# Performance work log

Hardware: AMD Instinct MI355X
Metric: run time of the kernel (lower is better)

## Reference

```python
import jax, jax.numpy as jnp
import numpy as np

B, N, F, R, DEG, STEPS = 4, 1024, 128, 16, 16, 2


def setup_inputs() -> dict:
    key = jax.random.key(0)
    ks = jax.random.split(key, 12)
    BN = B * N
    E = BN * DEG

    def edges(k):
        # edges kept within each graph of size N, then offset per graph
        e = jax.random.randint(k, (2, E), 0, N)
        off = jnp.repeat(jnp.arange(B, dtype=jnp.int32) * N, N * DEG)
        return e + off[None, :]

    return {
        "x_s": jax.random.normal(ks[0], (BN, F), jnp.float32),
        "edge_index_s": edges(ks[1]),
        "x_t": jax.random.normal(ks[2], (BN, F), jnp.float32),
        "edge_index_t": edges(ks[3]),
        "W1_self": jax.random.normal(ks[4], (F, F), jnp.float32) / np.float32(np.sqrt(F)),
        "W1_nbr": jax.random.normal(ks[5], (F, F), jnp.float32) / np.float32(np.sqrt(F)),
        "b1": jnp.zeros((F,), jnp.float32),
        "W2_self": jax.random.normal(ks[6], (R, R), jnp.float32) / np.float32(np.sqrt(R)),
        "W2_nbr": jax.random.normal(ks[7], (R, R), jnp.float32) / np.float32(np.sqrt(R)),
        "b2": jnp.zeros((R,), jnp.float32),
        "Wm1": jax.random.normal(ks[8], (R, R), jnp.float32) / np.float32(np.sqrt(R)),
        "bm1": jnp.zeros((R,), jnp.float32),
        "Wm2": jax.random.normal(ks[9], (R, 1), jnp.float32) / np.float32(np.sqrt(R)),
        "bm2": jnp.zeros((1,), jnp.float32),
        "r_steps": jax.random.normal(ks[10], (STEPS, B, N, R), jnp.float32),
    }


def _psi(x, ei, Ws, Wn, b):
    # simple GraphConv: self transform + summed neighbor transform
    agg = jax.ops.segment_sum(x[ei[0]], ei[1], num_segments=x.shape[0])
    return jax.nn.relu(x @ Ws + agg @ Wn + b)


def reference(x_s, edge_index_s, x_t, edge_index_t, W1_self, W1_nbr, b1,
              W2_self, W2_nbr, b2, Wm1, bm1, Wm2, bm2, r_steps):
    # psi_1 on both graphs, then dense-batch to [B, N, F] (equal-size graphs,
    # so masks are all-True and masked_softmax == softmax)
    h_s = _psi(x_s, edge_index_s, W1_self, W1_nbr, b1).reshape(B, N, F)
    h_t = _psi(x_t, edge_index_t, W1_self, W1_nbr, b1).reshape(B, N, F)

    S_hat = jnp.einsum('bsf,btf->bst', h_s, h_t)  # [B, Ns, Nt]
    S_0 = jax.nn.softmax(S_hat, axis=-1)

    for i in range(STEPS):
        S = jax.nn.softmax(S_hat, axis=-1)
        r_s = r_steps[i]                             # [B, N, R]
        r_t = jnp.einsum('bst,bsr->btr', S, r_s)     # S^T @ r_s
        o_s = _psi(r_s.reshape(B * N, R), edge_index_s, W2_self, W2_nbr, b2).reshape(B, N, R)
        o_t = _psi(r_t.reshape(B * N, R), edge_index_t, W2_self, W2_nbr, b2).reshape(B, N, R)
        D = o_s[:, :, None, :] - o_t[:, None, :, :]  # [B, Ns, Nt, R]
        upd = (jax.nn.relu(D @ Wm1 + bm1) @ Wm2 + bm2)[..., 0]
        S_hat = S_hat + upd

    S_L = jax.nn.softmax(S_hat, axis=-1)
    return (S_0, S_L)
```

## Files before the change

kernel.cpp:

```cpp
#include <hip/hip_runtime.h>

#define B_ 4
#define N_ 1024
#define F_ 128
#define R_ 16
#define E_ 65536
#define BN_ 4096

__global__ __launch_bounds__(256) void hist_k(
    const int* __restrict__ eis, const int* __restrict__ eit, int* __restrict__ counts) {
  const int* ei = blockIdx.y ? eit : eis;
  int* c = counts + blockIdx.y * BN_;
  int e = blockIdx.x * 256 + threadIdx.x;
  atomicAdd(c + ei[E_ + e], 1);
}

__global__ __launch_bounds__(256) void csr_scan(
    const int* __restrict__ counts, int* __restrict__ offs, int* __restrict__ cursor) {
  const int* c = counts + blockIdx.x * BN_;
  int* o = offs + blockIdx.x * (BN_ + 1);
  int* cur = cursor + blockIdx.x * BN_;
  int tid = threadIdx.x;
  int base = tid * 16;
  int local[16], sum = 0;
#pragma unroll
  for (int i = 0; i < 16; i++) { local[i] = sum; sum += c[base + i]; }
  __shared__ int csum[256];
  csum[tid] = sum;
  __syncthreads();
  for (int d = 1; d < 256; d <<= 1) {
    int v = (tid >= d) ? csum[tid - d] : 0;
    __syncthreads();
    csum[tid] += v;
    __syncthreads();
  }
  int prev = (tid == 0) ? 0 : csum[tid - 1];
#pragma unroll
  for (int i = 0; i < 16; i++) { int off = prev + local[i]; o[base + i] = off; cur[base + i] = off; }
  if (tid == 255) o[BN_] = csum[255];
}

__global__ __launch_bounds__(256) void csr_fill(
    const int* __restrict__ eis, const int* __restrict__ eit,
    int* __restrict__ cursor, int* __restrict__ csr) {
  const int* ei = blockIdx.y ? eit : eis;
  int* cur = cursor + blockIdx.y * BN_;
  int* cs = csr + blockIdx.y * E_;
  int e = blockIdx.x * 256 + threadIdx.x;
  int src = ei[e], dst = ei[E_ + e];
  int pos = atomicAdd(cur + dst, 1);
  cs[pos] = src;
}

__global__ __launch_bounds__(256) void gather_f(
    const float* __restrict__ xs, const float* __restrict__ xt,
    const int* __restrict__ csr, const int* __restrict__ offs,
    float* __restrict__ aggs, float* __restrict__ aggt) {
  const float* x = blockIdx.y ? xt : xs;
  const int* cs = csr + blockIdx.y * E_;
  const int* of = offs + blockIdx.y * (BN_ + 1);
  float* agg = blockIdx.y ? aggt : aggs;
  int node = blockIdx.x * 2 + (threadIdx.x >> 7);
  int ch = threadIdx.x & 127;
  int j0 = of[node], j1 = of[node + 1];
  float a0 = 0.f, a1 = 0.f, a2 = 0.f, a3 = 0.f;
  int j = j0;
  for (; j + 3 < j1; j += 4) {
    int s0 = cs[j], s1 = cs[j + 1], s2 = cs[j + 2], s3 = cs[j + 3];
    a0 += x[(size_t)s0 * F_ + ch];
    a1 += x[(size_t)s1 * F_ + ch];
    a2 += x[(size_t)s2 * F_ + ch];
    a3 += x[(size_t)s3 * F_ + ch];
  }
  for (; j < j1; j++) a0 += x[(size_t)cs[j] * F_ + ch];
  agg[(size_t)node * F_ + ch] = (a0 + a1) + (a2 + a3);
}

__global__ __launch_bounds__(256) void psi1_gemm(
    const float* __restrict__ xs, const float* __restrict__ aggs,
    const float* __restrict__ xt, const float* __restrict__ aggt,
    const float* __restrict__ Ws, const float* __restrict__ Wn,
    const float* __restrict__ bias, float* __restrict__ hs, float* __restrict__ ht) {
  const float* x   = blockIdx.z ? xt   : xs;
  const float* agg = blockIdx.z ? aggt : aggs;
  float*       h   = blockIdx.z ? ht   : hs;
  int n0 = blockIdx.x * 64, m0 = blockIdx.y * 64;
  int tid = threadIdx.x, tx = tid & 15, ty = tid >> 4;
  __shared__ __align__(16) float sA[16][68];
  __shared__ __align__(16) float sB[16][68];
  float acc[4][4] = {};
  for (int phase = 0; phase < 2; phase++) {
    const float* A  = phase ? agg : x;
    const float* Bw = phase ? Wn  : Ws;
    for (int kb = 0; kb < F_; kb += 16) {
      int row = tid >> 2, k4 = (tid & 3) * 4;
      float4 va = *(const float4*)(A + (size_t)(m0 + row) * F_ + kb + k4);
      sA[k4 + 0][row] = va.x; sA[k4 + 1][row] = va.y;
      sA[k4 + 2][row] = va.z; sA[k4 + 3][row] = va.w;
      int k = tid >> 4, n4 = (tid & 15) * 4;
      *(float4*)&sB[k][n4] = *(const float4*)(Bw + (size_t)(kb + k) * F_ + n0 + n4);
      __syncthreads();
#pragma unroll
      for (int kk = 0; kk < 16; kk++) {
        float a[4], bb[4];
        *(float4*)a  = *(const float4*)&sA[kk][ty * 4];
        *(float4*)bb = *(const float4*)&sB[kk][tx * 4];
#pragma unroll
        for (int i = 0; i < 4; i++)
#pragma unroll
          for (int j = 0; j < 4; j++) acc[i][j] += a[i] * bb[j];
      }
      __syncthreads();
    }
  }
  float4 bv = *(const float4*)(bias + n0 + tx * 4);
  float bj[4] = {bv.x, bv.y, bv.z, bv.w};
#pragma unroll
  for (int i = 0; i < 4; i++) {
    int m = m0 + ty * 4 + i;
    float4 o;
    o.x = fmaxf(acc[i][0] + bj[0], 0.f); o.y = fmaxf(acc[i][1] + bj[1], 0.f);
    o.z = fmaxf(acc[i][2] + bj[2], 0.f); o.w = fmaxf(acc[i][3] + bj[3], 0.f);
    *(float4*)(h + (size_t)m * F_ + n0 + tx * 4) = o;
  }
}

__global__ __launch_bounds__(256) void shat_gemm(
    const float* __restrict__ hs, const float* __restrict__ ht, float* __restrict__ S) {
  int b = blockIdx.z;
  int n0 = blockIdx.x * 128, m0 = blockIdx.y * 128;
  int tid = threadIdx.x, tx = tid & 15, ty = tid >> 4;
  __shared__ __align__(16) float sA[16][132];
  __shared__ __align__(16) float sB[16][132];
  float acc[8][8] = {};
  const float* Ag = hs + (size_t)(b * N_ + m0) * F_;
  const float* Bg = ht + (size_t)(b * N_ + n0) * F_;
  for (int kb = 0; kb < F_; kb += 16) {
#pragma unroll
    for (int l = 0; l < 2; l++) {
      int idx = tid + l * 256;
      int row = idx >> 2, k4 = (idx & 3) * 4;
      float4 va = *(const float4*)(Ag + (size_t)row * F_ + kb + k4);
      sA[k4 + 0][row] = va.x; sA[k4 + 1][row] = va.y;
      sA[k4 + 2][row] = va.z; sA[k4 + 3][row] = va.w;
      float4 vb = *(const float4*)(Bg + (size_t)row * F_ + kb + k4);
      sB[k4 + 0][row] = vb.x; sB[k4 + 1][row] = vb.y;
      sB[k4 + 2][row] = vb.z; sB[k4 + 3][row] = vb.w;
    }
    __syncthreads();
#pragma unroll
    for (int kk = 0; kk < 16; kk++) {
      float a[8], bb[8];
      *(float4*)&a[0]  = *(const float4*)&sA[kk][ty * 8];
      *(float4*)&a[4]  = *(const float4*)&sA[kk][ty * 8 + 4];
      *(float4*)&bb[0] = *(const float4*)&sB[kk][tx * 8];
      *(float4*)&bb[4] = *(const float4*)&sB[kk][tx * 8 + 4];
#pragma unroll
      for (int i = 0; i < 8; i++)
#pragma unroll
        for (int j = 0; j < 8; j++) acc[i][j] += a[i] * bb[j];
    }
    __syncthreads();
  }
#pragma unroll
  for (int i = 0; i < 8; i++) {
    size_t off = ((size_t)(b * N_ + m0 + ty * 8 + i)) * N_ + n0 + tx * 8;
    float4 o0 = {acc[i][0], acc[i][1], acc[i][2], acc[i][3]};
    float4 o1 = {acc[i][4], acc[i][5], acc[i][6], acc[i][7]};
    *(float4*)(S + off) = o0; *(float4*)(S + off + 4) = o1;
  }
}

__global__ __launch_bounds__(256) void softmax_row(
    const float* __restrict__ in, float* __restrict__ out) {
  int row = blockIdx.x;
  float4 v = ((const float4*)(in + (size_t)row * N_))[threadIdx.x];
  float m = fmaxf(fmaxf(v.x, v.y), fmaxf(v.z, v.w));
#pragma unroll
  for (int o = 32; o > 0; o >>= 1) m = fmaxf(m, __shfl_down(m, o, 64));
  __shared__ float rmax[4], rsum[4];
  int wave = threadIdx.x >> 6, lane = threadIdx.x & 63;
  if (lane == 0) rmax[wave] = m;
  __syncthreads();
  m = fmaxf(fmaxf(rmax[0], rmax[1]), fmaxf(rmax[2], rmax[3]));
  float e0 = __expf(v.x - m), e1 = __expf(v.y - m);
  float e2 = __expf(v.z - m), e3 = __expf(v.w - m);
  float s = e0 + e1 + e2 + e3;
#pragma unroll
  for (int o = 32; o > 0; o >>= 1) s += __shfl_down(s, o, 64);
  if (lane == 0) rsum[wave] = s;
  __syncthreads();
  s = rsum[0] + rsum[1] + rsum[2] + rsum[3];
  float inv = 1.f / s;
  float4 o4 = {e0 * inv, e1 * inv, e2 * inv, e3 * inv};
  ((float4*)(out + (size_t)row * N_))[threadIdx.x] = o4;
}

template <bool EXP>
__global__ __launch_bounds__(256) void rt_part_k(
    const float* __restrict__ S, const float2* __restrict__ stats,
    const float* __restrict__ rs, float* __restrict__ part) {
  int b = blockIdx.z, c = blockIdx.y, t0 = blockIdx.x * 256;
  int tid = threadIdx.x;
  int s0 = c * 32;
  __shared__ float rsh[32][16];
  __shared__ float sstat[64];
  if (tid < 128) {
    int srow = tid >> 2, c4 = (tid & 3) * 4;
    float4 v = *(const float4*)(rs + ((size_t)(b * N_ + s0 + srow)) * R_ + c4);
    rsh[srow][c4] = v.x; rsh[srow][c4 + 1] = v.y;
    rsh[srow][c4 + 2] = v.z; rsh[srow][c4 + 3] = v.w;
  } else if (EXP && tid < 192) {
    sstat[tid - 128] = ((const float*)(stats + b * N_ + s0))[tid - 128];
  }
  __syncthreads();
  float acc[16] = {};
  const float* Sp = S + ((size_t)(b * N_ + s0)) * N_ + t0 + tid;
#pragma unroll
  for (int s = 0; s < 32; s++) {
    float sv = Sp[(size_t)s * N_];
    if (EXP) sv = __expf(sv - sstat[2 * s]) * sstat[2 * s + 1];
#pragma unroll
    for (int r = 0; r < 16; r++) acc[r] += sv * rsh[s][r];
  }
  float* o = part + ((size_t)((b * 32 + c) * N_) + t0 + tid) * R_;
  *(float4*)(o + 0)  = *(float4*)&acc[0];
  *(float4*)(o + 4)  = *(float4*)&acc[4];
  *(float4*)(o + 8)  = *(float4*)&acc[8];
  *(float4*)(o + 12) = *(float4*)&acc[12];
}

__global__ __launch_bounds__(256) void rt_reduce(
    const float* __restrict__ part, float* __restrict__ rt) {
  int gid = blockIdx.x * 256 + threadIdx.x;
  int b = gid >> 12, tr = gid & 4095;
  const float* p = part + (size_t)b * (32 * N_ * R_) + (size_t)tr * 4;
  float4 acc = {0.f, 0.f, 0.f, 0.f};
#pragma unroll
  for (int c = 0; c < 32; c++) {
    float4 v = *(const float4*)(p + (size_t)c * (N_ * R_));
    acc.x += v.x; acc.y += v.y; acc.z += v.z; acc.w += v.w;
  }
  ((float4*)rt)[gid] = acc;
}

__global__ __launch_bounds__(256) void gpsi2p(
    const float* __restrict__ vs, const float* __restrict__ vt,
    const int* __restrict__ csr, const int* __restrict__ offs,
    const float* __restrict__ W2s, const float* __restrict__ W2n,
    const float* __restrict__ b2, const float* __restrict__ Wm1,
    float* __restrict__ Ps, float* __restrict__ Pt4) {
  const float* v = blockIdx.y ? vt : vs;
  const int* cs = csr + blockIdx.y * E_;
  const int* of = offs + blockIdx.y * (BN_ + 1);
  int col = threadIdx.x & 15, row = threadIdx.x >> 4;
  int node = blockIdx.x * 16 + row;
  int j0 = of[node], j1 = of[node + 1];
  float a0 = 0.f, a1 = 0.f, a2 = 0.f, a3 = 0.f;
  int j = j0;
  for (; j + 3 < j1; j += 4) {
    int s0 = cs[j], s1 = cs[j + 1], s2 = cs[j + 2], s3 = cs[j + 3];
    a0 += v[(size_t)s0 * R_ + col];
    a1 += v[(size_t)s1 * R_ + col];
    a2 += v[(size_t)s2 * R_ + col];
    a3 += v[(size_t)s3 * R_ + col];
  }
  for (; j < j1; j++) a0 += v[(size_t)cs[j] * R_ + col];
  __shared__ float sWs[16][16], sWn[16][16], sWm[16][17];
  __shared__ float sv[16][17], sa[16][17], so[16][17];
  sWs[row][col] = W2s[row * 16 + col];
  sWn[row][col] = W2n[row * 16 + col];
  sWm[row][col] = Wm1[row * 16 + col];
  sv[row][col] = v[(size_t)node * R_ + col];
  sa[row][col] = (a0 + a1) + (a2 + a3);
  __syncthreads();
  float o = b2[col];
#pragma unroll
  for (int k = 0; k < 16; k++) o += sv[row][k] * sWs[k][col] + sa[row][k] * sWn[k][col];
  so[row][col] = fmaxf(o, 0.f);
  __syncthreads();
  float p = 0;
#pragma unroll
  for (int k = 0; k < 16; k++) p += so[row][k] * sWm[k][col];
  if (blockIdx.y) {
    Pt4[((size_t)(col >> 2) * BN_ + node) * 4 + (col & 3)] = p;
  } else {
    Ps[(size_t)node * R_ + col] = p;
  }
}

template <int LAST>
__global__ __launch_bounds__(256) void upd_row3(
    float* __restrict__ Shat, const float* __restrict__ Ps, const float* __restrict__ Pt4,
    const float* __restrict__ bm1, const float* __restrict__ Wm2,
    const float* __restrict__ bm2, float2* __restrict__ stats, float* __restrict__ SL) {
  int b = blockIdx.y, s = blockIdx.x;
  int tid = threadIdx.x;
  __shared__ float sc[16], sw[16];
  __shared__ float wred[4];
  if (tid < 16) {
    sc[tid] = Ps[((size_t)(b * N_ + s)) * R_ + tid] + bm1[tid];
    sw[tid] = Wm2[tid];
  }
  float bm2v = bm2[0];
  __syncthreads();
  const size_t rowoff = (size_t)(b * N_ + s) * N_;
  float vals[4];
#pragma unroll
  for (int tile = 0; tile < 4; tile++) {
    int gt = b * N_ + tile * 256 + tid;
    float pt[16];
    *(float4*)&pt[0]  = *(const float4*)(Pt4 + ((size_t)0 * BN_ + gt) * 4);
    *(float4*)&pt[4]  = *(const float4*)(Pt4 + ((size_t)1 * BN_ + gt) * 4);
    *(float4*)&pt[8]  = *(const float4*)(Pt4 + ((size_t)2 * BN_ + gt) * 4);
    *(float4*)&pt[12] = *(const float4*)(Pt4 + ((size_t)3 * BN_ + gt) * 4);
    float sh = Shat[rowoff + tile * 256 + tid];
    float sum = bm2v;
#pragma unroll
    for (int r = 0; r < 16; r++) sum += fmaxf(sc[r] - pt[r], 0.f) * sw[r];
    float vv = sh + sum;
    vals[tile] = vv;
    if (!LAST) Shat[rowoff + tile * 256 + tid] = vv;
  }
  int wave = tid >> 6, lane = tid & 63;
  float m = fmaxf(fmaxf(vals[0], vals[1]), fmaxf(vals[2], vals[3]));
#pragma unroll
  for (int o = 32; o > 0; o >>= 1) m = fmaxf(m, __shfl_down(m, o, 64));
  if (lane == 0) wred[wave] = m;
  __syncthreads();
  m = fmaxf(fmaxf(wred[0], wred[1]), fmaxf(wred[2], wred[3]));
  __syncthreads();
  float e0 = __expf(vals[0] - m), e1 = __expf(vals[1] - m);
  float e2 = __expf(vals[2] - m), e3 = __expf(vals[3] - m);
  float l = (e0 + e1) + (e2 + e3);
#pragma unroll
  for (int o = 32; o > 0; o >>= 1) l += __shfl_down(l, o, 64);
  if (lane == 0) wred[wave] = l;
  __syncthreads();
  l = (wred[0] + wred[1]) + (wred[2] + wred[3]);
  if (LAST) {
    float inv = 1.f / l;
    SL[rowoff + 0 * 256 + tid] = e0 * inv;
    SL[rowoff + 1 * 256 + tid] = e1 * inv;
    SL[rowoff + 2 * 256 + tid] = e2 * inv;
    SL[rowoff + 3 * 256 + tid] = e3 * inv;
  } else {
    if (tid == 0) stats[b * N_ + s] = make_float2(m, 1.f / l);
  }
}

extern "C" void kernel_launch(void* const* d_in, const int* in_sizes, int n_in,
                              void* d_out, int out_size, void* d_ws, size_t ws_size,
                              hipStream_t stream) {
  const float* x_s = (const float*)d_in[0];
  const int*   ei_s = (const int*)d_in[1];
  const float* x_t = (const float*)d_in[2];
  const int*   ei_t = (const int*)d_in[3];
  const float* W1s = (const float*)d_in[4];
  const float* W1n = (const float*)d_in[5];
  const float* b1  = (const float*)d_in[6];
  const float* W2s = (const float*)d_in[7];
  const float* W2n = (const float*)d_in[8];
  const float* b2  = (const float*)d_in[9];
  const float* Wm1 = (const float*)d_in[10];
  const float* bm1 = (const float*)d_in[11];
  const float* Wm2 = (const float*)d_in[12];
  const float* bm2 = (const float*)d_in[13];
  const float* r_steps = (const float*)d_in[14];

  float* out = (float*)d_out;
  float* S0 = out;
  float* SL = out + (size_t)B_ * N_ * N_;

  float* ws = (float*)d_ws;
  float* agg_s = ws;
  float* agg_t = ws + 524288;
  float* h_s   = ws + 1048576;
  float* h_t   = ws + 1572864;
  float* part  = ws;
  float* Shat  = ws + 2097152;
  float* rtb   = ws + 6291456;
  float2* stats = (float2*)(ws + 6356992);
  float* Ps    = ws + 6488064;
  float* Pt4   = ws + 6553600;
  int* counts  = (int*)(ws + 6619136);
  int* cursor  = (int*)(ws + 6627328);
  int* offs    = (int*)(ws + 6635520);
  int* csr     = (int*)(ws + 6643720);

  hipMemsetAsync(counts, 0, 2 * BN_ * sizeof(int), stream);
  hist_k<<<dim3(E_ / 256, 2), 256, 0, stream>>>(ei_s, ei_t, counts);
  csr_scan<<<2, 256, 0, stream>>>(counts, offs, cursor);
  csr_fill<<<dim3(E_ / 256, 2), 256, 0, stream>>>(ei_s, ei_t, cursor, csr);

  gather_f<<<dim3(BN_ / 2, 2), 256, 0, stream>>>(x_s, x_t, csr, offs, agg_s, agg_t);
  psi1_gemm<<<dim3(2, 64, 2), 256, 0, stream>>>(x_s, agg_s, x_t, agg_t, W1s, W1n, b1, h_s, h_t);

  shat_gemm<<<dim3(8, 8, 4), 256, 0, stream>>>(h_s, h_t, Shat);
  softmax_row<<<B_ * N_, 256, 0, stream>>>(Shat, S0);

  const float* rs0 = r_steps;
  rt_part_k<false><<<dim3(4, 32, 4), 256, 0, stream>>>(S0, nullptr, rs0, part);
  rt_reduce<<<64, 256, 0, stream>>>(part, rtb);
  gpsi2p<<<dim3(256, 2), 256, 0, stream>>>(rs0, rtb, csr, offs, W2s, W2n, b2, Wm1, Ps, Pt4);
  upd_row3<0><<<dim3(N_, B_), 256, 0, stream>>>(Shat, Ps, Pt4, bm1, Wm2, bm2, stats, nullptr);

  const float* rs1 = r_steps + (size_t)B_ * N_ * R_;
  rt_part_k<true><<<dim3(4, 32, 4), 256, 0, stream>>>(Shat, stats, rs1, part);
  rt_reduce<<<64, 256, 0, stream>>>(part, rtb);
  gpsi2p<<<dim3(256, 2), 256, 0, stream>>>(rs1, rtb, csr, offs, W2s, W2n, b2, Wm1, Ps, Pt4);
  upd_row3<1><<<dim3(N_, B_), 256, 0, stream>>>(Shat, Ps, Pt4, bm1, Wm2, bm2, nullptr, SL);
}
```

Measured before the change: 230.5 us.

## Merge CSR build and refinement steps into cooperative persistent kernels

Replaces the memset, histogram, scan and fill launches with one cooperative kernel that uses grid-wide syncs between phases. The two refinement steps (rt partials, reduce, psi2 projection, row update) become a single persistent cooperative kernel of 256 blocks, each looping over tasks. The aim is to remove many kernel launch gaps. In exchange, the refinement work runs on only 256 blocks with several grid barriers, so parallelism drops, especially in the row-update phase where each block handles 16 rows in sequence.

Result: slower. 686.8 us (+197.9%).

```diff
diff --git a/kernel.cpp b/kernel.cpp
--- a/kernel.cpp
+++ b/kernel.cpp
@@ -1,4 +1,7 @@
 #include <hip/hip_runtime.h>
+#include <hip/hip_cooperative_groups.h>
+
+namespace cg = cooperative_groups;
 
 #define B_ 4
 #define N_ 1024
@@ -7,49 +10,51 @@
 #define E_ 65536
 #define BN_ 4096
 
-__global__ __launch_bounds__(256) void hist_k(
-    const int* __restrict__ eis, const int* __restrict__ eit, int* __restrict__ counts) {
-  const int* ei = blockIdx.y ? eit : eis;
-  int* c = counts + blockIdx.y * BN_;
-  int e = blockIdx.x * 256 + threadIdx.x;
-  atomicAdd(c + ei[E_ + e], 1);
-}
-
-__global__ __launch_bounds__(256) void csr_scan(
-    const int* __restrict__ counts, int* __restrict__ offs, int* __restrict__ cursor) {
-  const int* c = counts + blockIdx.x * BN_;
-  int* o = offs + blockIdx.x * (BN_ + 1);
-  int* cur = cursor + blockIdx.x * BN_;
-  int tid = threadIdx.x;
-  int base = tid * 16;
-  int local[16], sum = 0;
-#pragma unroll
-  for (int i = 0; i < 16; i++) { local[i] = sum; sum += c[base + i]; }
-  __shared__ int csum[256];
-  csum[tid] = sum;
-  __syncthreads();
-  for (int d = 1; d < 256; d <<= 1) {
-    int v = (tid >= d) ? csum[tid - d] : 0;
+__global__ __launch_bounds__(256) void csr_coop(
+    const int* __restrict__ eis, const int* __restrict__ eit,
+    int* __restrict__ counts, int* __restrict__ cursor,
+    int* __restrict__ offs, int* __restrict__ csr) {
+  cg::grid_group grid = cg::this_grid();
+  int blk = blockIdx.x, tid = threadIdx.x;
+  int gid = blk * 256 + tid;
+  if (gid < 2 * BN_) counts[gid] = 0;
+  grid.sync();
+  {
+    int g = gid >> 16, e = gid & 65535;
+    const int* ei = g ? eit : eis;
+    atomicAdd(counts + g * BN_ + ei[E_ + e], 1);
+  }
+  grid.sync();
+  if (blk < 2) {
+    const int* c = counts + blk * BN_;
+    int* o = offs + blk * (BN_ + 1);
+    int* cur = cursor + blk * BN_;
+    int base = tid * 16;
+    int local[16], sum = 0;
+#pragma unroll
+    for (int i = 0; i < 16; i++) { local[i] = sum; sum += c[base + i]; }
+    __shared__ int csum[256];
+    csum[tid] = sum;
     __syncthreads();
-    csum[tid] += v;
-    __syncthreads();
-  }
-  int prev = (tid == 0) ? 0 : csum[tid - 1];
-#pragma unroll
-  for (int i = 0; i < 16; i++) { int off = prev + local[i]; o[base + i] = off; cur[base + i] = off; }
-  if (tid == 255) o[BN_] = csum[255];
-}
-
-__global__ __launch_bounds__(256) void csr_fill(
-    const int* __restrict__ eis, const int* __restrict__ eit,
-    int* __restrict__ cursor, int* __restrict__ csr) {
-  const int* ei = blockIdx.y ? eit : eis;
-  int* cur = cursor + blockIdx.y * BN_;
-  int* cs = csr + blockIdx.y * E_;
-  int e = blockIdx.x * 256 + threadIdx.x;
-  int src = ei[e], dst = ei[E_ + e];
-  int pos = atomicAdd(cur + dst, 1);
-  cs[pos] = src;
+    for (int d = 1; d < 256; d <<= 1) {
+      int v = (tid >= d) ? csum[tid - d] : 0;
+      __syncthreads();
+      csum[tid] += v;
+      __syncthreads();
+    }
+    int prev = (tid == 0) ? 0 : csum[tid - 1];
+#pragma unroll
+    for (int i = 0; i < 16; i++) { int off = prev + local[i]; o[base + i] = off; cur[base + i] = off; }
+    if (tid == 255) o[BN_] = csum[255];
+  }
+  grid.sync();
+  {
+    int g = gid >> 16, e = gid & 65535;
+    const int* ei = g ? eit : eis;
+    int src = ei[e], dst = ei[E_ + e];
+    int pos = atomicAdd(cursor + g * BN_ + dst, 1);
+    csr[g * E_ + pos] = src;
+  }
 }
 
 __global__ __launch_bounds__(256) void gather_f(
@@ -196,156 +201,179 @@
   ((float4*)(out + (size_t)row * N_))[threadIdx.x] = o4;
 }
 
-template <bool EXP>
-__global__ __launch_bounds__(256) void rt_part_k(
-    const float* __restrict__ S, const float2* __restrict__ stats,
-    const float* __restrict__ rs, float* __restrict__ part) {
-  int b = blockIdx.z, c = blockIdx.y, t0 = blockIdx.x * 256;
-  int tid = threadIdx.x;
-  int s0 = c * 32;
-  __shared__ float rsh[32][16];
-  __shared__ float sstat[64];
-  if (tid < 128) {
-    int srow = tid >> 2, c4 = (tid & 3) * 4;
-    float4 v = *(const float4*)(rs + ((size_t)(b * N_ + s0 + srow)) * R_ + c4);
-    rsh[srow][c4] = v.x; rsh[srow][c4 + 1] = v.y;
-    rsh[srow][c4 + 2] = v.z; rsh[srow][c4 + 3] = v.w;
-  } else if (EXP && tid < 192) {
-    sstat[tid - 128] = ((const float*)(stats + b * N_ + s0))[tid - 128];
-  }
-  __syncthreads();
-  float acc[16] = {};
-  const float* Sp = S + ((size_t)(b * N_ + s0)) * N_ + t0 + tid;
-#pragma unroll
-  for (int s = 0; s < 32; s++) {
-    float sv = Sp[(size_t)s * N_];
-    if (EXP) sv = __expf(sv - sstat[2 * s]) * sstat[2 * s + 1];
-#pragma unroll
-    for (int r = 0; r < 16; r++) acc[r] += sv * rsh[s][r];
-  }
-  float* o = part + ((size_t)((b * 32 + c) * N_) + t0 + tid) * R_;
-  *(float4*)(o + 0)  = *(float4*)&acc[0];
-  *(float4*)(o + 4)  = *(float4*)&acc[4];
-  *(float4*)(o + 8)  = *(float4*)&acc[8];
-  *(float4*)(o + 12) = *(float4*)&acc[12];
-}
-
-__global__ __launch_bounds__(256) void rt_reduce(
-    const float* __restrict__ part, float* __restrict__ rt) {
-  int gid = blockIdx.x * 256 + threadIdx.x;
-  int b = gid >> 12, tr = gid & 4095;
-  const float* p = part + (size_t)b * (32 * N_ * R_) + (size_t)tr * 4;
-  float4 acc = {0.f, 0.f, 0.f, 0.f};
-#pragma unroll
-  for (int c = 0; c < 32; c++) {
-    float4 v = *(const float4*)(p + (size_t)c * (N_ * R_));
-    acc.x += v.x; acc.y += v.y; acc.z += v.z; acc.w += v.w;
-  }
-  ((float4*)rt)[gid] = acc;
-}
-
-__global__ __launch_bounds__(256) void gpsi2p(
-    const float* __restrict__ vs, const float* __restrict__ vt,
+__global__ __launch_bounds__(256, 2) void refine_coop(
+    const float* __restrict__ S0, float* __restrict__ Shat,
+    const float* __restrict__ r_steps,
     const int* __restrict__ csr, const int* __restrict__ offs,
     const float* __restrict__ W2s, const float* __restrict__ W2n,
     const float* __restrict__ b2, const float* __restrict__ Wm1,
-    float* __restrict__ Ps, float* __restrict__ Pt4) {
-  const float* v = blockIdx.y ? vt : vs;
-  const int* cs = csr + blockIdx.y * E_;
-  const int* of = offs + blockIdx.y * (BN_ + 1);
-  int col = threadIdx.x & 15, row = threadIdx.x >> 4;
-  int node = blockIdx.x * 16 + row;
-  int j0 = of[node], j1 = of[node + 1];
-  float a0 = 0.f, a1 = 0.f, a2 = 0.f, a3 = 0.f;
-  int j = j0;
-  for (; j + 3 < j1; j += 4) {
-    int s0 = cs[j], s1 = cs[j + 1], s2 = cs[j + 2], s3 = cs[j + 3];
-    a0 += v[(size_t)s0 * R_ + col];
-    a1 += v[(size_t)s1 * R_ + col];
-    a2 += v[(size_t)s2 * R_ + col];
-    a3 += v[(size_t)s3 * R_ + col];
-  }
-  for (; j < j1; j++) a0 += v[(size_t)cs[j] * R_ + col];
+    const float* __restrict__ bm1, const float* __restrict__ Wm2,
+    const float* __restrict__ bm2,
+    float* __restrict__ part, float* __restrict__ rtb,
+    float* __restrict__ Ps, float* __restrict__ Pt4,
+    float2* __restrict__ stats, float* __restrict__ SL) {
+  cg::grid_group grid = cg::this_grid();
+  int blk = blockIdx.x, tid = threadIdx.x;
+  __shared__ float rsh[32][16];
+  __shared__ float sstat[64];
   __shared__ float sWs[16][16], sWn[16][16], sWm[16][17];
   __shared__ float sv[16][17], sa[16][17], so[16][17];
-  sWs[row][col] = W2s[row * 16 + col];
-  sWn[row][col] = W2n[row * 16 + col];
-  sWm[row][col] = Wm1[row * 16 + col];
-  sv[row][col] = v[(size_t)node * R_ + col];
-  sa[row][col] = (a0 + a1) + (a2 + a3);
-  __syncthreads();
-  float o = b2[col];
-#pragma unroll
-  for (int k = 0; k < 16; k++) o += sv[row][k] * sWs[k][col] + sa[row][k] * sWn[k][col];
-  so[row][col] = fmaxf(o, 0.f);
-  __syncthreads();
-  float p = 0;
-#pragma unroll
-  for (int k = 0; k < 16; k++) p += so[row][k] * sWm[k][col];
-  if (blockIdx.y) {
-    Pt4[((size_t)(col >> 2) * BN_ + node) * 4 + (col & 3)] = p;
-  } else {
-    Ps[(size_t)node * R_ + col] = p;
-  }
-}
-
-template <int LAST>
-__global__ __launch_bounds__(256) void upd_row3(
-    float* __restrict__ Shat, const float* __restrict__ Ps, const float* __restrict__ Pt4,
-    const float* __restrict__ bm1, const float* __restrict__ Wm2,
-    const float* __restrict__ bm2, float2* __restrict__ stats, float* __restrict__ SL) {
-  int b = blockIdx.y, s = blockIdx.x;
-  int tid = threadIdx.x;
-  __shared__ float sc[16], sw[16];
+  __shared__ float sc16[16], sw16[16];
   __shared__ float wred[4];
-  if (tid < 16) {
-    sc[tid] = Ps[((size_t)(b * N_ + s)) * R_ + tid] + bm1[tid];
-    sw[tid] = Wm2[tid];
-  }
-  float bm2v = bm2[0];
-  __syncthreads();
-  const size_t rowoff = (size_t)(b * N_ + s) * N_;
-  float vals[4];
-#pragma unroll
-  for (int tile = 0; tile < 4; tile++) {
-    int gt = b * N_ + tile * 256 + tid;
-    float pt[16];
-    *(float4*)&pt[0]  = *(const float4*)(Pt4 + ((size_t)0 * BN_ + gt) * 4);
-    *(float4*)&pt[4]  = *(const float4*)(Pt4 + ((size_t)1 * BN_ + gt) * 4);
-    *(float4*)&pt[8]  = *(const float4*)(Pt4 + ((size_t)2 * BN_ + gt) * 4);
-    *(float4*)&pt[12] = *(const float4*)(Pt4 + ((size_t)3 * BN_ + gt) * 4);
-    float sh = Shat[rowoff + tile * 256 + tid];
-    float sum = bm2v;
-#pragma unroll
-    for (int r = 0; r < 16; r++) sum += fmaxf(sc[r] - pt[r], 0.f) * sw[r];
-    float vv = sh + sum;
-    vals[tile] = vv;
-    if (!LAST) Shat[rowoff + tile * 256 + tid] = vv;
-  }
   int wave = tid >> 6, lane = tid & 63;
-  float m = fmaxf(fmaxf(vals[0], vals[1]), fmaxf(vals[2], vals[3]));
-#pragma unroll
-  for (int o = 32; o > 0; o >>= 1) m = fmaxf(m, __shfl_down(m, o, 64));
-  if (lane == 0) wred[wave] = m;
-  __syncthreads();
-  m = fmaxf(fmaxf(wred[0], wred[1]), fmaxf(wred[2], wred[3]));
-  __syncthreads();
-  float e0 = __expf(vals[0] - m), e1 = __expf(vals[1] - m);
-  float e2 = __expf(vals[2] - m), e3 = __expf(vals[3] - m);
-  float l = (e0 + e1) + (e2 + e3);
-#pragma unroll
-  for (int o = 32; o > 0; o >>= 1) l += __shfl_down(l, o, 64);
-  if (lane == 0) wred[wave] = l;
-  __syncthreads();
-  l = (wred[0] + wred[1]) + (wred[2] + wred[3]);
-  if (LAST) {
-    float inv = 1.f / l;
-    SL[rowoff + 0 * 256 + tid] = e0 * inv;
-    SL[rowoff + 1 * 256 + tid] = e1 * inv;
-    SL[rowoff + 2 * 256 + tid] = e2 * inv;
-    SL[rowoff + 3 * 256 + tid] = e3 * inv;
-  } else {
-    if (tid == 0) stats[b * N_ + s] = make_float2(m, 1.f / l);
+
+  for (int step = 0; step < 2; step++) {
+    const float* rs = r_steps + (size_t)step * BN_ * R_;
+
+    for (int it = 0; it < 2; it++) {
+      int task = blk + it * 256;
+      int b = task >> 7, c = (task >> 2) & 31, t0 = (task & 3) * 256;
+      int s0 = c * 32;
+      __syncthreads();
+      if (tid < 128) {
+        int srow = tid >> 2, c4 = (tid & 3) * 4;
+        float4 v = *(const float4*)(rs + ((size_t)(b * N_ + s0 + srow)) * R_ + c4);
+        rsh[srow][c4] = v.x; rsh[srow][c4 + 1] = v.y;
+        rsh[srow][c4 + 2] = v.z; rsh[srow][c4 + 3] = v.w;
+      } else if (step == 1 && tid < 192) {
+        sstat[tid - 128] = ((const float*)(stats + b * N_ + s0))[tid - 128];
+      }
+      __syncthreads();
+      float acc[16] = {};
+      const float* Sp = ((step == 0) ? S0 : Shat) + ((size_t)(b * N_ + s0)) * N_ + t0 + tid;
+      if (step == 0) {
+#pragma unroll
+        for (int s = 0; s < 32; s++) {
+          float p = Sp[(size_t)s * N_];
+#pragma unroll
+          for (int r = 0; r < 16; r++) acc[r] += p * rsh[s][r];
+        }
+      } else {
+#pragma unroll
+        for (int s = 0; s < 32; s++) {
+          float p = __expf(Sp[(size_t)s * N_] - sstat[2 * s]) * sstat[2 * s + 1];
+#pragma unroll
+          for (int r = 0; r < 16; r++) acc[r] += p * rsh[s][r];
+        }
+      }
+      float* o = part + ((size_t)((b * 32 + c) * N_) + t0 + tid) * R_;
+      *(float4*)(o + 0)  = *(float4*)&acc[0];
+      *(float4*)(o + 4)  = *(float4*)&acc[4];
+      *(float4*)(o + 8)  = *(float4*)&acc[8];
+      *(float4*)(o + 12) = *(float4*)&acc[12];
+    }
+    grid.sync();
+
+    if (blk < 64) {
+      int gid = blk * 256 + tid;
+      int b = gid >> 12, tr = gid & 4095;
+      const float* p = part + (size_t)b * (32 * N_ * R_) + (size_t)tr * 4;
+      float4 acc = {0.f, 0.f, 0.f, 0.f};
+#pragma unroll
+      for (int c = 0; c < 32; c++) {
+        float4 v = *(const float4*)(p + (size_t)c * (N_ * R_));
+        acc.x += v.x; acc.y += v.y; acc.z += v.z; acc.w += v.w;
+      }
+      ((float4*)rtb)[gid] = acc;
+    }
+    grid.sync();
+
+    for (int it = 0; it < 2; it++) {
+      int task = blk + it * 256;
+      int gy = task >> 8, bx = task & 255;
+      const float* v = gy ? rtb : rs;
+      const int* cs = csr + gy * E_;
+      const int* of = offs + gy * (BN_ + 1);
+      int col = tid & 15, row = tid >> 4;
+      int node = bx * 16 + row;
+      int j0 = of[node], j1 = of[node + 1];
+      float a0 = 0.f, a1 = 0.f, a2 = 0.f, a3 = 0.f;
+      int j = j0;
+      for (; j + 3 < j1; j += 4) {
+        int s0 = cs[j], s1 = cs[j + 1], s2 = cs[j + 2], s3 = cs[j + 3];
+        a0 += v[(size_t)s0 * R_ + col];
+        a1 += v[(size_t)s1 * R_ + col];
+        a2 += v[(size_t)s2 * R_ + col];
+        a3 += v[(size_t)s3 * R_ + col];
+      }
+      for (; j < j1; j++) a0 += v[(size_t)cs[j] * R_ + col];
+      __syncthreads();
+      sWs[row][col] = W2s[row * 16 + col];
+      sWn[row][col] = W2n[row * 16 + col];
+      sWm[row][col] = Wm1[row * 16 + col];
+      sv[row][col] = v[(size_t)node * R_ + col];
+      sa[row][col] = (a0 + a1) + (a2 + a3);
+      __syncthreads();
+      float o = b2[col];
+#pragma unroll
+      for (int k = 0; k < 16; k++) o += sv[row][k] * sWs[k][col] + sa[row][k] * sWn[k][col];
+      so[row][col] = fmaxf(o, 0.f);
+      __syncthreads();
+      float p = 0;
+#pragma unroll
+      for (int k = 0; k < 16; k++) p += so[row][k] * sWm[k][col];
+      if (gy) {
+        Pt4[((size_t)(col >> 2) * BN_ + node) * 4 + (col & 3)] = p;
+      } else {
+        Ps[(size_t)node * R_ + col] = p;
+      }
+    }
+    grid.sync();
+
+    float bm2v = bm2[0];
+    for (int i = 0; i < 16; i++) {
+      int task = blk * 16 + i;
+      int b = task >> 10, s = task & 1023;
+      __syncthreads();
+      if (tid < 16) {
+        sc16[tid] = Ps[((size_t)(b * N_ + s)) * R_ + tid] + bm1[tid];
+        sw16[tid] = Wm2[tid];
+      }
+      __syncthreads();
+      const size_t rowoff = (size_t)(b * N_ + s) * N_;
+      float vals[4];
+#pragma unroll
+      for (int tile = 0; tile < 4; tile++) {
+        int gt = b * N_ + tile * 256 + tid;
+        float pt[16];
+        *(float4*)&pt[0]  = *(const float4*)(Pt4 + ((size_t)0 * BN_ + gt) * 4);
+        *(float4*)&pt[4]  = *(const float4*)(Pt4 + ((size_t)1 * BN_ + gt) * 4);
+        *(float4*)&pt[8]  = *(const float4*)(Pt4 + ((size_t)2 * BN_ + gt) * 4);
+        *(float4*)&pt[12] = *(const float4*)(Pt4 + ((size_t)3 * BN_ + gt) * 4);
+        float sh = Shat[rowoff + tile * 256 + tid];
+        float sum = bm2v;
+#pragma unroll
+        for (int r = 0; r < 16; r++) sum += fmaxf(sc16[r] - pt[r], 0.f) * sw16[r];
+        float vv = sh + sum;
+        vals[tile] = vv;
+        if (step == 0) Shat[rowoff + tile * 256 + tid] = vv;
+      }
+      float m = fmaxf(fmaxf(vals[0], vals[1]), fmaxf(vals[2], vals[3]));
+#pragma unroll
+      for (int o = 32; o > 0; o >>= 1) m = fmaxf(m, __shfl_down(m, o, 64));
+      if (lane == 0) wred[wave] = m;
+      __syncthreads();
+      m = fmaxf(fmaxf(wred[0], wred[1]), fmaxf(wred[2], wred[3]));
+      __syncthreads();
+      float e0 = __expf(vals[0] - m), e1 = __expf(vals[1] - m);
+      float e2 = __expf(vals[2] - m), e3 = __expf(vals[3] - m);
+      float l = (e0 + e1) + (e2 + e3);
+#pragma unroll
+      for (int o = 32; o > 0; o >>= 1) l += __shfl_down(l, o, 64);
+      if (lane == 0) wred[wave] = l;
+      __syncthreads();
+      l = (wred[0] + wred[1]) + (wred[2] + wred[3]);
+      if (step == 1) {
+        float inv = 1.f / l;
+        SL[rowoff + 0 * 256 + tid] = e0 * inv;
+        SL[rowoff + 1 * 256 + tid] = e1 * inv;
+        SL[rowoff + 2 * 256 + tid] = e2 * inv;
+        SL[rowoff + 3 * 256 + tid] = e3 * inv;
+      } else {
+        if (tid == 0) stats[b * N_ + s] = make_float2(m, 1.f / l);
+      }
+    }
+    if (step == 0) grid.sync();
   }
 }
 
@@ -388,10 +416,11 @@
   int* offs    = (int*)(ws + 6635520);
   int* csr     = (int*)(ws + 6643720);
 
-  hipMemsetAsync(counts, 0, 2 * BN_ * sizeof(int), stream);
-  hist_k<<<dim3(E_ / 256, 2), 256, 0, stream>>>(ei_s, ei_t, counts);
-  csr_scan<<<2, 256, 0, stream>>>(counts, offs, cursor);
-  csr_fill<<<dim3(E_ / 256, 2), 256, 0, stream>>>(ei_s, ei_t, cursor, csr);
+  {
+    void* args[] = {(void*)&ei_s, (void*)&ei_t, (void*)&counts, (void*)&cursor,
+                    (void*)&offs, (void*)&csr};
+    hipLaunchCooperativeKernel((const void*)csr_coop, dim3(512), dim3(256), args, 0, stream);
+  }
 
   gather_f<<<dim3(BN_ / 2, 2), 256, 0, stream>>>(x_s, x_t, csr, offs, agg_s, agg_t);
   psi1_gemm<<<dim3(2, 64, 2), 256, 0, stream>>>(x_s, agg_s, x_t, agg_t, W1s, W1n, b1, h_s, h_t);
@@ -399,15 +428,11 @@
   shat_gemm<<<dim3(8, 8, 4), 256, 0, stream>>>(h_s, h_t, Shat);
   softmax_row<<<B_ * N_, 256, 0, stream>>>(Shat, S0);
 
-  const float* rs0 = r_steps;
-  rt_part_k<false><<<dim3(4, 32, 4), 256, 0, stream>>>(S0, nullptr, rs0, part);
-  rt_reduce<<<64, 256, 0, stream>>>(part, rtb);
-  gpsi2p<<<dim3(256, 2), 256, 0, stream>>>(rs0, rtb, csr, offs, W2s, W2n, b2, Wm1, Ps, Pt4);
-  upd_row3<0><<<dim3(N_, B_), 256, 0, stream>>>(Shat, Ps, Pt4, bm1, Wm2, bm2, stats, nullptr);
-
-  const float* rs1 = r_steps + (size_t)B_ * N_ * R_;
-  rt_part_k<true><<<dim3(4, 32, 4), 256, 0, stream>>>(Shat, stats, rs1, part);
-  rt_reduce<<<64, 256, 0, stream>>>(part, rtb);
-  gpsi2p<<<dim3(256, 2), 256, 0, stream>>>(rs1, rtb, csr, offs, W2s, W2n, b2, Wm1, Ps, Pt4);
-  upd_row3<1><<<dim3(N_, B_), 256, 0, stream>>>(Shat, Ps, Pt4, bm1, Wm2, bm2, nullptr, SL);
-}
+  {
+    void* args[] = {(void*)&S0, (void*)&Shat, (void*)&r_steps, (void*)&csr, (void*)&offs,
+                    (void*)&W2s, (void*)&W2n, (void*)&b2, (void*)&Wm1, (void*)&bm1,
+                    (void*)&Wm2, (void*)&bm2, (void*)&part, (void*)&rtb, (void*)&Ps,
+                    (void*)&Pt4, (void*)&stats, (void*)&SL};
+    hipLaunchCooperativeKernel((const void*)refine_coop, dim3(256), dim3(256), args, 0, stream);
+  }
+}
```

## Fuse initial softmax into rt_part, vectorize gather, process two rows per update block

Applied to the files above, without the earlier changes.

Replaces the initial softmax kernel with a stats-only pass and computes the normalized S0 inside rt_part_k, writing it out while accumulating S^T r. This avoids re-reading a stored S0 from memory. Also vectorizes the feature gather with float4 loads across 8 nodes per block, and makes the update kernel handle two rows per block to reuse Pt4 loads. The cost is extra exp work in rt_part and higher register pressure in the update kernel.

New measurement: 243.3 us. 5.5% more time.

```diff
diff --git a/kernel.cpp b/kernel.cpp
--- a/kernel.cpp
+++ b/kernel.cpp
@@ -60,20 +60,32 @@
   const int* cs = csr + blockIdx.y * E_;
   const int* of = offs + blockIdx.y * (BN_ + 1);
   float* agg = blockIdx.y ? aggt : aggs;
-  int node = blockIdx.x * 2 + (threadIdx.x >> 7);
-  int ch = threadIdx.x & 127;
+  int node = blockIdx.x * 8 + (threadIdx.x >> 5);
+  int ch4 = (threadIdx.x & 31) * 4;
   int j0 = of[node], j1 = of[node + 1];
-  float a0 = 0.f, a1 = 0.f, a2 = 0.f, a3 = 0.f;
+  float4 a0 = {0, 0, 0, 0}, a1 = {0, 0, 0, 0}, a2 = {0, 0, 0, 0}, a3 = {0, 0, 0, 0};
   int j = j0;
   for (; j + 3 < j1; j += 4) {
     int s0 = cs[j], s1 = cs[j + 1], s2 = cs[j + 2], s3 = cs[j + 3];
-    a0 += x[(size_t)s0 * F_ + ch];
-    a1 += x[(size_t)s1 * F_ + ch];
-    a2 += x[(size_t)s2 * F_ + ch];
-    a3 += x[(size_t)s3 * F_ + ch];
-  }
-  for (; j < j1; j++) a0 += x[(size_t)cs[j] * F_ + ch];
-  agg[(size_t)node * F_ + ch] = (a0 + a1) + (a2 + a3);
+    float4 v0 = *(const float4*)(x + (size_t)s0 * F_ + ch4);
+    float4 v1 = *(const float4*)(x + (size_t)s1 * F_ + ch4);
+    float4 v2 = *(const float4*)(x + (size_t)s2 * F_ + ch4);
+    float4 v3 = *(const float4*)(x + (size_t)s3 * F_ + ch4);
+    a0.x += v0.x; a0.y += v0.y; a0.z += v0.z; a0.w += v0.w;
+    a1.x += v1.x; a1.y += v1.y; a1.z += v1.z; a1.w += v1.w;
+    a2.x += v2.x; a2.y += v2.y; a2.z += v2.z; a2.w += v2.w;
+    a3.x += v3.x; a3.y += v3.y; a3.z += v3.z; a3.w += v3.w;
+  }
+  for (; j < j1; j++) {
+    float4 v = *(const float4*)(x + (size_t)cs[j] * F_ + ch4);
+    a0.x += v.x; a0.y += v.y; a0.z += v.z; a0.w += v.w;
+  }
+  float4 o;
+  o.x = (a0.x + a1.x) + (a2.x + a3.x);
+  o.y = (a0.y + a1.y) + (a2.y + a3.y);
+  o.z = (a0.z + a1.z) + (a2.z + a3.z);
+  o.w = (a0.w + a1.w) + (a2.w + a3.w);
+  *(float4*)(agg + (size_t)node * F_ + ch4) = o;
 }
 
 __global__ __launch_bounds__(256) void psi1_gemm(
@@ -171,8 +183,8 @@
   }
 }
 
-__global__ __launch_bounds__(256) void softmax_row(
-    const float* __restrict__ in, float* __restrict__ out) {
+__global__ __launch_bounds__(256) void row_stats(
+    const float* __restrict__ in, float2* __restrict__ stats) {
   int row = blockIdx.x;
   float4 v = ((const float4*)(in + (size_t)row * N_))[threadIdx.x];
   float m = fmaxf(fmaxf(v.x, v.y), fmaxf(v.z, v.w));
@@ -183,23 +195,21 @@
   if (lane == 0) rmax[wave] = m;
   __syncthreads();
   m = fmaxf(fmaxf(rmax[0], rmax[1]), fmaxf(rmax[2], rmax[3]));
-  float e0 = __expf(v.x - m), e1 = __expf(v.y - m);
-  float e2 = __expf(v.z - m), e3 = __expf(v.w - m);
-  float s = e0 + e1 + e2 + e3;
+  float s = __expf(v.x - m) + __expf(v.y - m) + __expf(v.z - m) + __expf(v.w - m);
 #pragma unroll
   for (int o = 32; o > 0; o >>= 1) s += __shfl_down(s, o, 64);
   if (lane == 0) rsum[wave] = s;
   __syncthreads();
-  s = rsum[0] + rsum[1] + rsum[2] + rsum[3];
-  float inv = 1.f / s;
-  float4 o4 = {e0 * inv, e1 * inv, e2 * inv, e3 * inv};
-  ((float4*)(out + (size_t)row * N_))[threadIdx.x] = o4;
-}
-
-template <bool EXP>
+  if (threadIdx.x == 0) {
+    float tot = rsum[0] + rsum[1] + rsum[2] + rsum[3];
+    stats[row] = make_float2(m, 1.f / tot);
+  }
+}
+
+template <bool WRITE_S>
 __global__ __launch_bounds__(256) void rt_part_k(
     const float* __restrict__ S, const float2* __restrict__ stats,
-    const float* __restrict__ rs, float* __restrict__ part) {
+    const float* __restrict__ rs, float* __restrict__ part, float* __restrict__ Sout) {
   int b = blockIdx.z, c = blockIdx.y, t0 = blockIdx.x * 256;
   int tid = threadIdx.x;
   int s0 = c * 32;
@@ -210,18 +220,20 @@
     float4 v = *(const float4*)(rs + ((size_t)(b * N_ + s0 + srow)) * R_ + c4);
     rsh[srow][c4] = v.x; rsh[srow][c4 + 1] = v.y;
     rsh[srow][c4 + 2] = v.z; rsh[srow][c4 + 3] = v.w;
-  } else if (EXP && tid < 192) {
+  } else if (tid < 192) {
     sstat[tid - 128] = ((const float*)(stats + b * N_ + s0))[tid - 128];
   }
   __syncthreads();
   float acc[16] = {};
-  const float* Sp = S + ((size_t)(b * N_ + s0)) * N_ + t0 + tid;
+  const size_t base = ((size_t)(b * N_ + s0)) * N_ + t0 + tid;
+  const float* Sp = S + base;
+  float* So = WRITE_S ? (Sout + base) : nullptr;
 #pragma unroll
   for (int s = 0; s < 32; s++) {
-    float sv = Sp[(size_t)s * N_];
-    if (EXP) sv = __expf(sv - sstat[2 * s]) * sstat[2 * s + 1];
-#pragma unroll
-    for (int r = 0; r < 16; r++) acc[r] += sv * rsh[s][r];
+    float p = __expf(Sp[(size_t)s * N_] - sstat[2 * s]) * sstat[2 * s + 1];
+    if (WRITE_S) So[(size_t)s * N_] = p;
+#pragma unroll
+    for (int r = 0; r < 16; r++) acc[r] += p * rsh[s][r];
   }
   float* o = part + ((size_t)((b * 32 + c) * N_) + t0 + tid) * R_;
   *(float4*)(o + 0)  = *(float4*)&acc[0];
@@ -290,22 +302,20 @@
 }
 
 template <int LAST>
-__global__ __launch_bounds__(256) void upd_row3(
+__global__ __launch_bounds__(256) void upd_row4(
     float* __restrict__ Shat, const float* __restrict__ Ps, const float* __restrict__ Pt4,
     const float* __restrict__ bm1, const float* __restrict__ Wm2,
     const float* __restrict__ bm2, float2* __restrict__ stats, float* __restrict__ SL) {
-  int b = blockIdx.y, s = blockIdx.x;
+  int b = blockIdx.y, s0 = blockIdx.x * 2;
   int tid = threadIdx.x;
-  __shared__ float sc[16], sw[16];
-  __shared__ float wred[4];
-  if (tid < 16) {
-    sc[tid] = Ps[((size_t)(b * N_ + s)) * R_ + tid] + bm1[tid];
-    sw[tid] = Wm2[tid];
-  }
+  __shared__ float sc[2][16], sw16[16];
+  __shared__ float wred[2][4];
+  if (tid < 32) sc[tid >> 4][tid & 15] =
+      Ps[((size_t)(b * N_ + s0 + (tid >> 4))) * R_ + (tid & 15)] + bm1[tid & 15];
+  if (tid < 16) sw16[tid] = Wm2[tid];
   float bm2v = bm2[0];
   __syncthreads();
-  const size_t rowoff = (size_t)(b * N_ + s) * N_;
-  float vals[4];
+  float vals[2][4];
 #pragma unroll
   for (int tile = 0; tile < 4; tile++) {
     int gt = b * N_ + tile * 256 + tid;
@@ -314,38 +324,55 @@
     *(float4*)&pt[4]  = *(const float4*)(Pt4 + ((size_t)1 * BN_ + gt) * 4);
     *(float4*)&pt[8]  = *(const float4*)(Pt4 + ((size_t)2 * BN_ + gt) * 4);
     *(float4*)&pt[12] = *(const float4*)(Pt4 + ((size_t)3 * BN_ + gt) * 4);
-    float sh = Shat[rowoff + tile * 256 + tid];
-    float sum = bm2v;
-#pragma unroll
-    for (int r = 0; r < 16; r++) sum += fmaxf(sc[r] - pt[r], 0.f) * sw[r];
-    float vv = sh + sum;
-    vals[tile] = vv;
-    if (!LAST) Shat[rowoff + tile * 256 + tid] = vv;
+#pragma unroll
+    for (int rr = 0; rr < 2; rr++) {
+      size_t off = ((size_t)(b * N_ + s0 + rr)) * N_ + tile * 256 + tid;
+      float sum = bm2v;
+#pragma unroll
+      for (int r = 0; r < 16; r++) sum += fmaxf(sc[rr][r] - pt[r], 0.f) * sw16[r];
+      float vv = Shat[off] + sum;
+      vals[rr][tile] = vv;
+      if (!LAST) Shat[off] = vv;
+    }
   }
   int wave = tid >> 6, lane = tid & 63;
-  float m = fmaxf(fmaxf(vals[0], vals[1]), fmaxf(vals[2], vals[3]));
-#pragma unroll
-  for (int o = 32; o > 0; o >>= 1) m = fmaxf(m, __shfl_down(m, o, 64));
-  if (lane == 0) wred[wave] = m;
-  __syncthreads();
-  m = fmaxf(fmaxf(wred[0], wred[1]), fmaxf(wred[2], wred[3]));
-  __syncthreads();
-  float e0 = __expf(vals[0] - m), e1 = __expf(vals[1] - m);
-  float e2 = __expf(vals[2] - m), e3 = __expf(vals[3] - m);
-  float l = (e0 + e1) + (e2 + e3);
-#pragma unroll
-  for (int o = 32; o > 0; o >>= 1) l += __shfl_down(l, o, 64);
-  if (lane == 0) wred[wave] = l;
-  __syncthreads();
-  l = (wred[0] + wred[1]) + (wred[2] + wred[3]);
-  if (LAST) {
-    float inv = 1.f / l;
-    SL[rowoff + 0 * 256 + tid] = e0 * inv;
-    SL[rowoff + 1 * 256 + tid] = e1 * inv;
-    SL[rowoff + 2 * 256 + tid] = e2 * inv;
-    SL[rowoff + 3 * 256 + tid] = e3 * inv;
-  } else {
-    if (tid == 0) stats[b * N_ + s] = make_float2(m, 1.f / l);
+#pragma unroll
+  for (int rr = 0; rr < 2; rr++) {
+    float m = fmaxf(fmaxf(vals[rr][0], vals[rr][1]), fmaxf(vals[rr][2], vals[rr][3]));
+#pragma unroll
+    for (int o = 32; o > 0; o >>= 1) m = fmaxf(m, __shfl_down(m, o, 64));
+    if (lane == 0) wred[rr][wave] = m;
+  }
+  __syncthreads();
+  float M[2];
+#pragma unroll
+  for (int rr = 0; rr < 2; rr++)
+    M[rr] = fmaxf(fmaxf(wred[rr][0], wred[rr][1]), fmaxf(wred[rr][2], wred[rr][3]));
+  __syncthreads();
+  float e[2][4];
+#pragma unroll
+  for (int rr = 0; rr < 2; rr++) {
+    e[rr][0] = __expf(vals[rr][0] - M[rr]); e[rr][1] = __expf(vals[rr][1] - M[rr]);
+    e[rr][2] = __expf(vals[rr][2] - M[rr]); e[rr][3] = __expf(vals[rr][3] - M[rr]);
+    float l = (e[rr][0] + e[rr][1]) + (e[rr][2] + e[rr][3]);
+#pragma unroll
+    for (int o = 32; o > 0; o >>= 1) l += __shfl_down(l, o, 64);
+    if (lane == 0) wred[rr][wave] = l;
+  }
+  __syncthreads();
+#pragma unroll
+  for (int rr = 0; rr < 2; rr++) {
+    float l = (wred[rr][0] + wred[rr][1]) + (wred[rr][2] + wred[rr][3]);
+    size_t rowoff = ((size_t)(b * N_ + s0 + rr)) * N_;
+    if (LAST) {
+      float inv = 1.f / l;
+      SL[rowoff + 0 * 256 + tid] = e[rr][0] * inv;
+      SL[rowoff + 1 * 256 + tid] = e[rr][1] * inv;
+      SL[rowoff + 2 * 256 + tid] = e[rr][2] * inv;
+      SL[rowoff + 3 * 256 + tid] = e[rr][3] * inv;
+    } else {
+      if (tid == 0) stats[b * N_ + s0 + rr] = make_float2(M[rr], 1.f / l);
+    }
   }
 }
 
@@ -393,21 +420,21 @@
   csr_scan<<<2, 256, 0, stream>>>(counts, offs, cursor);
   csr_fill<<<dim3(E_ / 256, 2), 256, 0, stream>>>(ei_s, ei_t, cursor, csr);
 
-  gather_f<<<dim3(BN_ / 2, 2), 256, 0, stream>>>(x_s, x_t, csr, offs, agg_s, agg_t);
+  gather_f<<<dim3(BN_ / 8, 2), 256, 0, stream>>>(x_s, x_t, csr, offs, agg_s, agg_t);
   psi1_gemm<<<dim3(2, 64, 2), 256, 0, stream>>>(x_s, agg_s, x_t, agg_t, W1s, W1n, b1, h_s, h_t);
 
   shat_gemm<<<dim3(8, 8, 4), 256, 0, stream>>>(h_s, h_t, Shat);
-  softmax_row<<<B_ * N_, 256, 0, stream>>>(Shat, S0);
+  row_stats<<<B_ * N_, 256, 0, stream>>>(Shat, stats);
 
   const float* rs0 = r_steps;
-  rt_part_k<false><<<dim3(4, 32, 4), 256, 0, stream>>>(S0, nullptr, rs0, part);
+  rt_part_k<true><<<dim3(4, 32, 4), 256, 0, stream>>>(Shat, stats, rs0, part, S0);
   rt_reduce<<<64, 256, 0, stream>>>(part, rtb);
   gpsi2p<<<dim3(256, 2), 256, 0, stream>>>(rs0, rtb, csr, offs, W2s, W2n, b2, Wm1, Ps, Pt4);
-  upd_row3<0><<<dim3(N_, B_), 256, 0, stream>>>(Shat, Ps, Pt4, bm1, Wm2, bm2, stats, nullptr);
+  upd_row4<0><<<dim3(N_ / 2, B_), 256, 0, stream>>>(Shat, Ps, Pt4, bm1, Wm2, bm2, stats, nullptr);
 
   const float* rs1 = r_steps + (size_t)B_ * N_ * R_;
-  rt_part_k<true><<<dim3(4, 32, 4), 256, 0, stream>>>(Shat, stats, rs1, part);
+  rt_part_k<false><<<dim3(4, 32, 4), 256, 0, stream>>>(Shat, stats, rs1, part, nullptr);
   rt_reduce<<<64, 256, 0, stream>>>(part, rtb);
   gpsi2p<<<dim3(256, 2), 256, 0, stream>>>(rs1, rtb, csr, offs, W2s, W2n, b2, Wm1, Ps, Pt4);
-  upd_row3<1><<<dim3(N_, B_), 256, 0, stream>>>(Shat, Ps, Pt4, bm1, Wm2, bm2, nullptr, SL);
-}
+  upd_row4<1><<<dim3(N_ / 2, B_), 256, 0, stream>>>(Shat, Ps, Pt4, bm1, Wm2, bm2, nullptr, SL);
+}
```
